# Optimization experiments

Hardware: AMD Instinct MI355X
Metric: run time of the kernel (lower is better)

## Reference

```python
import jax, jax.numpy as jnp
import numpy as np

DIM = 1024
HEADS = 16
DIM_HEAD = 64
INNER = HEADS * DIM_HEAD
SCALE = DIM_HEAD ** -0.5


def setup_inputs() -> dict:
    key = jax.random.key(0)
    k1, k2, k3 = jax.random.split(key, 3)
    b, n = 2, 2048
    x = jax.random.normal(k1, (b, n, DIM), dtype=jnp.float32)
    mask = jnp.ones((b, n), dtype=bool)
    # to_qkv: Linear(dim, 3*inner, bias=False) stored as [dim, 3*inner]
    w_qkv = jax.random.normal(k2, (DIM, 3 * INNER), dtype=jnp.float32) * (DIM ** -0.5)
    # to_out: Linear(inner, dim, bias=False) stored as [inner, dim]
    w_out = jax.random.normal(k3, (INNER, DIM), dtype=jnp.float32) * (INNER ** -0.5)
    g = jnp.ones((DIM,), dtype=jnp.float32)  # LayerNorm gain
    return {"x": x, "mask": mask, "w_qkv": w_qkv, "w_out": w_out, "g": g}


def _layernorm(x, g):
    eps = 1e-5 if x.dtype == jnp.float32 else 1e-3
    mean = jnp.mean(x, axis=-1, keepdims=True)
    var = jnp.var(x, axis=-1, keepdims=True)  # unbiased=False
    return (x - mean) * jax.lax.rsqrt(var + eps) * g


def reference(x, mask, w_qkv, w_out, g):
    b, n, _ = x.shape
    qkv = x @ w_qkv  # [b, n, 3*inner]
    q, k, v = jnp.split(qkv, 3, axis=-1)
    # b n (h d) -> b h n d
    split_heads = lambda t: t.reshape(b, n, HEADS, DIM_HEAD).transpose(0, 2, 1, 3)
    q, k, v = split_heads(q), split_heads(k), split_heads(v)
    q = q * SCALE
    sim = jnp.einsum('bhid,bhjd->bhij', q, k)  # [b, h, n, n]
    mask_value = -jnp.finfo(sim.dtype).max
    key_mask = mask[:, None, None, :]  # b 1 1 j
    sim = jnp.where(key_mask, sim, mask_value)
    causal_mask = jnp.triu(jnp.ones((n, n), dtype=bool), k=1)
    sim = jnp.where(causal_mask, mask_value, sim)
    attn = jax.nn.softmax(sim.astype(jnp.float32), axis=-1).astype(sim.dtype)
    out = jnp.einsum('bhij,bhjd->bhid', attn, v)
    out = out.transpose(0, 2, 1, 3).reshape(b, n, INNER)  # b h n d -> b n (h d)
    out = out @ w_out
    return _layernorm(out, g)
```

## Files before the change

### kernel.cpp

```cpp
#include <hip/hip_runtime.h>
#include <hip/hip_bf16.h>


typedef __bf16 bf16_t;
typedef __bf16 bf16x8 __attribute__((ext_vector_type(8)));
typedef __bf16 bf16x4 __attribute__((ext_vector_type(4)));
typedef float  f32x4  __attribute__((ext_vector_type(4)));

#define DIMX   1024
#define HEADS  16
#define DHEAD  64
#define INNER  1024
#define SEQ    2048
#define BATCH  2
#define NROWS  (BATCH * SEQ)
#define QKV_N  (3 * INNER)
#define NQT    (SEQ / 64)
#define QK2SCALE 0.18033688011f

__device__ __forceinline__ bf16_t f2b(float f) { return (bf16_t)f; }

__device__ __forceinline__ float fexp2(float x) {
#if __has_builtin(__builtin_amdgcn_exp2f)
  return __builtin_amdgcn_exp2f(x);
#else
  return exp2f(x);
#endif
}

__device__ __forceinline__ void gload16(const bf16_t* g, bf16_t* s) {
  __builtin_amdgcn_global_load_lds(
      (const __attribute__((address_space(1))) unsigned int*)g,
      (__attribute__((address_space(3))) unsigned int*)s, 16, 0, 0);
}

__device__ __forceinline__ f32x4 mfma16(bf16x8 a, bf16x8 b, f32x4 c) {
  return __builtin_amdgcn_mfma_f32_16x16x32_bf16(a, b, c, 0, 0, 0);
}

__global__ __launch_bounds__(256)
void prep_all(const float* __restrict__ x, const float* __restrict__ w_qkv,
              const float* __restrict__ w_out, bf16_t* __restrict__ xb,
              bf16_t* __restrict__ wqkvT, bf16_t* __restrict__ woutT) {
  __shared__ float tile[32][33];
  const int bid = blockIdx.x;
  if (bid < 4096) {
    const int i = bid * 256 + threadIdx.x;
    float4 v = *(const float4*)&x[(size_t)i * 4];
    bf16x4 o;
    o[0] = f2b(v.x); o[1] = f2b(v.y); o[2] = f2b(v.z); o[3] = f2b(v.w);
    *(bf16x4*)&xb[(size_t)i * 4] = o;
    return;
  }
  const float* in; bf16_t* out; int R, C, bx, by;
  if (bid < 4096 + 3072) {
    const int t1 = bid - 4096;
    in = w_qkv; out = wqkvT; R = DIMX; C = QKV_N; bx = t1 % 96; by = t1 / 96;
  } else {
    const int t2 = bid - 7168;
    in = w_out; out = woutT; R = DIMX; C = DIMX; bx = t2 & 31; by = t2 >> 5;
  }
  const int c0 = bx * 32, r0 = by * 32;
  const int tx = threadIdx.x & 31, ty = threadIdx.x >> 5;
  #pragma unroll
  for (int i = 0; i < 32; i += 8)
    tile[ty + i][tx] = in[(size_t)(r0 + ty + i) * C + c0 + tx];
  __syncthreads();
  #pragma unroll
  for (int i = 0; i < 32; i += 8)
    out[(size_t)(c0 + ty + i) * R + r0 + tx] = f2b(tile[tx][ty + i]);
}

__global__ __launch_bounds__(256)
void vtrans(const bf16_t* __restrict__ qkv, bf16_t* __restrict__ vt) {
  __shared__ bf16_t t[64][66];
  const int bh = blockIdx.y;
  const int b = bh >> 4, h = bh & 15;
  const int j0 = blockIdx.x * 64;
  const int tx = threadIdx.x & 63, ty = threadIdx.x >> 6;
  #pragma unroll
  for (int i = 0; i < 64; i += 4)
    t[ty + i][tx] = qkv[(size_t)(b * SEQ + j0 + ty + i) * QKV_N + 2 * INNER + h * 64 + tx];
  __syncthreads();
  #pragma unroll
  for (int i = 0; i < 64; i += 4)
    vt[((size_t)bh * 64 + ty + i) * SEQ + j0 + tx] = t[tx][ty + i];
}

template<int OUT_F32>
__global__ __launch_bounds__(256)
void gemm_bt(const bf16_t* __restrict__ A, const bf16_t* __restrict__ Bt,
             void* __restrict__ Cp, int M, int N, int K) {
  constexpr int BK = 64;
  __shared__ bf16_t As[128 * BK];
  __shared__ bf16_t Bs[128 * BK];
  const int t = threadIdx.x;
  const int w = t >> 6, l = t & 63, lo = l & 15, hi = l >> 4;
  const int nwg = gridDim.x * gridDim.y;
  int flat = blockIdx.y * gridDim.x + blockIdx.x;
  if ((nwg & 7) == 0) flat = (flat & 7) * (nwg >> 3) + (flat >> 3);
  const int m0 = (flat / gridDim.x) * 128, n0 = (flat % gridDim.x) * 128;
  const int wm = (w >> 1) * 64, wn = (w & 1) * 64;
  const int sl  = l >> 3;
  const int sgc = ((l & 7) ^ sl) * 8;
  const int r7  = lo & 7;
  f32x4 acc[4][4] = {};
  for (int k0 = 0; k0 < K; k0 += BK) {
    #pragma unroll
    for (int c = 0; c < 4; ++c) {
      const int rb = w * 32 + c * 8;
      gload16(&A [(size_t)(m0 + rb + sl) * K + k0 + sgc], &As[rb * BK + l * 8]);
      gload16(&Bt[(size_t)(n0 + rb + sl) * K + k0 + sgc], &Bs[rb * BK + l * 8]);
    }
    __syncthreads();
    #pragma unroll
    for (int kk = 0; kk < 2; ++kk) {
      bf16x8 af[4], bfr[4];
      #pragma unroll
      for (int mi = 0; mi < 4; ++mi)
        af[mi] = *(const bf16x8*)&As[(wm + mi * 16 + lo) * BK +
                                     (((kk * 4 + hi) ^ r7) << 3)];
      #pragma unroll
      for (int nj = 0; nj < 4; ++nj)
        bfr[nj] = *(const bf16x8*)&Bs[(wn + nj * 16 + lo) * BK +
                                      (((kk * 4 + hi) ^ r7) << 3)];
      __builtin_amdgcn_s_setprio(1);
      #pragma unroll
      for (int mi = 0; mi < 4; ++mi)
        #pragma unroll
        for (int nj = 0; nj < 4; ++nj)
          acc[mi][nj] = mfma16(af[mi], bfr[nj], acc[mi][nj]);
      __builtin_amdgcn_s_setprio(0);
    }
    __syncthreads();
  }
  #pragma unroll
  for (int mi = 0; mi < 4; ++mi)
    #pragma unroll
    for (int nj = 0; nj < 4; ++nj)
      #pragma unroll
      for (int r = 0; r < 4; ++r) {
        size_t row = m0 + wm + mi * 16 + hi * 4 + r;
        size_t col = n0 + wn + nj * 16 + lo;
        if (OUT_F32)
          ((float*)Cp)[row * N + col] = acc[mi][nj][r];
        else
          ((bf16_t*)Cp)[row * N + col] = f2b(acc[mi][nj][r]);
      }
}

__global__ __launch_bounds__(256, 4)
void attn_fa12(const bf16_t* __restrict__ qkv, const bf16_t* __restrict__ vt,
               bf16_t* __restrict__ attn_out, bf16_t* __restrict__ pacc,
               float* __restrict__ plsum) {
  const int bx  = blockIdx.x;
  const int xcd = bx & 7, idx = bx >> 3;
  const int bh  = xcd * 4 + (idx & 3);
  const int ta  = (idx >> 2) & 15;
  const int half = idx >> 6;
  const int tb  = NQT - 1 - ta;
  const int b = bh >> 4, h = bh & 15;
  const int t = threadIdx.x, w = t >> 6, l = t & 63, lo = l & 15, hi = l >> 4;

  __shared__ bf16_t Ks[2][64 * 64];
  __shared__ bf16_t Vs[2][64 * 64];

  const int srow = l >> 3;
  const int sgc  = ((l & 7) ^ srow) * 8;
  const size_t kgbase = (size_t)(b * SEQ) * QKV_N + INNER + h * 64;
  const size_t vgbase = (size_t)bh * 64 * SEQ;

  auto STAGE = [&](int ti, int buf) {
    const int j0 = ti * 64;
    #pragma unroll
    for (int c = 0; c < 2; ++c) {
      const int rb = w * 16 + c * 8;
      gload16(&qkv[kgbase + (size_t)(j0 + rb + srow) * QKV_N + sgc],
              &Ks[buf][rb * 64]);
      gload16(&vt[vgbase + (size_t)(rb + srow) * SEQ + j0 + sgc],
              &Vs[buf][rb * 64]);
    }
  };

  const int r7 = lo & 7;
  bf16x8 vone8;
  #pragma unroll
  for (int i = 0; i < 8; ++i) vone8[i] = f2b(1.0f);
  f32x4 acc[4];
  f32x4 acc_l;

  auto SEG = [&](const int qt, const int t0, const int t1, const bool dmask) {
    const size_t qb = (size_t)(b * SEQ + qt * 64 + w * 16 + lo) * QKV_N + h * 64;
    bf16x8 qf0 = *(const bf16x8*)&qkv[qb + hi * 8];
    bf16x8 qf1 = *(const bf16x8*)&qkv[qb + 32 + hi * 8];
    #pragma unroll
    for (int i = 0; i < 8; ++i) {
      qf0[i] = f2b((float)qf0[i] * QK2SCALE);
      qf1[i] = f2b((float)qf1[i] * QK2SCALE);
    }
    const f32x4 fz = {};
    acc[0] = fz; acc[1] = fz; acc[2] = fz; acc[3] = fz;
    acc_l = fz;
    const int qrow = qt * 64 + w * 16 + lo;

    STAGE(t0, 0);
    for (int ti = t0; ti <= t1; ++ti) {
      const int buf = (ti - t0) & 1;
      __syncthreads();
      if (ti + 1 <= t1) STAGE(ti + 1, buf ^ 1);
      const bool mB = dmask && (ti == t1);
      __builtin_amdgcn_s_setprio(1);
      #pragma unroll
      for (int pr = 0; pr < 2; ++pr) {
        const int jb0 = pr * 2;
        if (!(mB && jb0 > w)) {
          bf16x8 pa;
          #pragma unroll
          for (int q = 0; q < 2; ++q) {
            const int jb = jb0 + q;
            f32x4 z = fz;
            if (!(mB && jb > w)) {
              const bf16_t* kp = &Ks[buf][(jb * 16 + lo) * 64];
              bf16x8 kf0 = *(const bf16x8*)&kp[(hi ^ r7) << 3];
              bf16x8 kf1 = *(const bf16x8*)&kp[((hi + 4) ^ r7) << 3];
              z = mfma16(kf0, qf0, z);
              z = mfma16(kf1, qf1, z);
            }
            #pragma unroll
            for (int r = 0; r < 4; ++r) {
              float pe = fexp2(z[r]);
              if (mB) {
                const int jglob = ti * 64 + jb * 16 + hi * 4 + r;
                if (jglob > qrow) pe = 0.f;
              }
              pa[q * 4 + r] = f2b(pe);
            }
          }
          #pragma unroll
          for (int dj = 0; dj < 4; ++dj) {
            const bf16_t* vp = &Vs[buf][(dj * 16 + lo) * 64];
            bf16x4 va = *(const bf16x4*)&vp[
                (((2 * jb0 + (hi >> 1)) ^ r7) << 3) + ((hi & 1) << 2)];
            bf16x4 vb = *(const bf16x4*)&vp[
                (((2 * jb0 + 2 + (hi >> 1)) ^ r7) << 3) + ((hi & 1) << 2)];
            bf16x8 vf;
            #pragma unroll
            for (int i = 0; i < 4; ++i) { vf[i] = va[i]; vf[i + 4] = vb[i]; }
            acc[dj] = mfma16(pa, vf, acc[dj]);
          }
          acc_l = mfma16(pa, vone8, acc_l);
        }
      }
      __builtin_amdgcn_s_setprio(0);
    }
    __syncthreads();
  };

  if (half == 0) {
    SEG(ta, 0, ta, true);
    #pragma unroll
    for (int r = 0; r < 4; ++r) {
      const float lr = 1.f / acc_l[r];
      #pragma unroll
      for (int dj = 0; dj < 4; ++dj)
        attn_out[(size_t)(b * SEQ + ta * 64 + w * 16 + hi * 4 + r) * INNER +
                 h * 64 + dj * 16 + lo] = f2b(acc[dj][r] * lr);
    }
    SEG(tb, 0, 15 - ta, false);
    {
      const int prb = (bh * 16 + (tb - 16)) * 64;
      #pragma unroll
      for (int dj = 0; dj < 4; ++dj)
        #pragma unroll
        for (int r = 0; r < 4; ++r)
          pacc[(size_t)(prb + w * 16 + hi * 4 + r) * 64 + dj * 16 + lo] =
              f2b(acc[dj][r]);
      if (lo == 0) {
        #pragma unroll
        for (int r = 0; r < 4; ++r)
          plsum[prb + w * 16 + hi * 4 + r] = acc_l[r];
      }
    }
  } else {
    SEG(tb, 16 - ta, tb, true);
    {
      const int prb = (bh * 16 + (tb - 16)) * 64;
      #pragma unroll
      for (int dj = 0; dj < 4; ++dj)
        #pragma unroll
        for (int r = 0; r < 4; ++r)
          pacc[2097152 + (size_t)(prb + w * 16 + hi * 4 + r) * 64 + dj * 16 + lo] =
              f2b(acc[dj][r]);
      if (lo == 0) {
        #pragma unroll
        for (int r = 0; r < 4; ++r)
          plsum[32768 + prb + w * 16 + hi * 4 + r] = acc_l[r];
      }
    }
  }
}

__global__ __launch_bounds__(256)
void attn_combine(const bf16_t* __restrict__ pacc, const float* __restrict__ plsum,
                  bf16_t* __restrict__ attn_out) {
  const int g = blockIdx.x * 256 + threadIdx.x;
  const int d8 = g & 7;
  const int row = g >> 3;
  const int qr = row & 63, qt = 16 + ((row >> 6) & 15), bh = row >> 10;
  const int b = bh >> 4, h = bh & 15;
  bf16x8 xa = *(const bf16x8*)&pacc[(size_t)row * 64 + d8 * 8];
  bf16x8 ya = *(const bf16x8*)&pacc[2097152 + (size_t)row * 64 + d8 * 8];
  const float inv = 1.f / (plsum[row] + plsum[32768 + row]);
  bf16x8 o;
  #pragma unroll
  for (int i = 0; i < 8; ++i)
    o[i] = f2b(((float)xa[i] + (float)ya[i]) * inv);
  *(bf16x8*)&attn_out[(size_t)(b * SEQ + qt * 64 + qr) * INNER + h * 64 + d8 * 8] = o;
}

__global__ __launch_bounds__(256)
void layernorm_b(const bf16_t* __restrict__ in, const float* __restrict__ g,
                 float* __restrict__ out) {
  const int row = blockIdx.x;
  const bf16_t* xr = in + (size_t)row * DIMX;
  const int c = threadIdx.x * 4;
  bf16x4 v4 = *(const bf16x4*)&xr[c];
  const float vx = (float)v4[0], vy = (float)v4[1], vz = (float)v4[2], vw = (float)v4[3];
  float s = vx + vy + vz + vw;
  float q = vx * vx + vy * vy + vz * vz + vw * vw;
  #pragma unroll
  for (int o = 32; o > 0; o >>= 1) {
    s += __shfl_down(s, o);
    q += __shfl_down(q, o);
  }
  __shared__ float rs[4], rq[4];
  const int wid = threadIdx.x >> 6;
  if ((threadIdx.x & 63) == 0) { rs[wid] = s; rq[wid] = q; }
  __syncthreads();
  s = rs[0] + rs[1] + rs[2] + rs[3];
  q = rq[0] + rq[1] + rq[2] + rq[3];
  const float mean = s * (1.f / DIMX);
  const float var  = q * (1.f / DIMX) - mean * mean;
  const float inv  = rsqrtf(var + 1e-5f);
  float4 gv = *(const float4*)&g[c];
  float4 o4;
  o4.x = (vx - mean) * inv * gv.x;
  o4.y = (vy - mean) * inv * gv.y;
  o4.z = (vz - mean) * inv * gv.z;
  o4.w = (vw - mean) * inv * gv.w;
  *(float4*)&out[(size_t)row * DIMX + c] = o4;
}

extern "C" void kernel_launch(void* const* d_in, const int* in_sizes, int n_in,
                              void* d_out, int out_size, void* d_ws, size_t ws_size,
                              hipStream_t stream) {
  const float* x     = (const float*)d_in[0];
  const float* w_qkv = (const float*)d_in[2];
  const float* w_out = (const float*)d_in[3];
  const float* g     = (const float*)d_in[4];

  char* ws = (char*)d_ws;
  const size_t MB = 1024 * 1024;
  bf16_t* xb     = (bf16_t*)(ws);
  bf16_t* wqkvT  = (bf16_t*)(ws + 8 * MB);
  bf16_t* woutT  = (bf16_t*)(ws + 14 * MB);
  bf16_t* qkv    = (bf16_t*)(ws + 16 * MB);
  bf16_t* vt     = (bf16_t*)(ws + 40 * MB);
  bf16_t* attn_o = (bf16_t*)(ws + 48 * MB);
  bf16_t* pacc   = (bf16_t*)(ws);
  float*  plsum  = (float*) (ws + 8 * MB);
  bf16_t* outpre = (bf16_t*)(ws + 16 * MB);

  prep_all<<<8192, 256, 0, stream>>>(x, w_qkv, w_out, xb, wqkvT, woutT);

  gemm_bt<0><<<dim3(QKV_N / 128, NROWS / 128), 256, 0, stream>>>(
      xb, wqkvT, qkv, NROWS, QKV_N, DIMX);

  vtrans<<<dim3(SEQ / 64, BATCH * HEADS), 256, 0, stream>>>(qkv, vt);

  attn_fa12<<<dim3(1024), 256, 0, stream>>>(qkv, vt, attn_o, pacc, plsum);
  attn_combine<<<dim3(1024), 256, 0, stream>>>(pacc, plsum, attn_o);

  gemm_bt<0><<<dim3(DIMX / 128, NROWS / 128), 256, 0, stream>>>(
      attn_o, woutT, outpre, NROWS, DIMX, DIMX);

  layernorm_b<<<NROWS, 256, 0, stream>>>(outpre, g, (float*)d_out);
}
```

Before: 112.4 us.

## Fuse V transpose into QKV GEMM epilogue and split-K the output projection

The QKV GEMM now writes V tiles transposed through shared memory straight into the vt buffer, which removes the separate vtrans kernel and its extra pass over V. The output projection is split into two K halves (grid z=2) so 512 workgroups run instead of 256, writing fp32 partials. LayerNorm then sums the two partials before normalizing. This trades one fewer launch and better occupancy for the projection against extra fp32 partial-buffer traffic (2x16MB write and read).

```diff
diff --git a/kernel.cpp b/kernel.cpp
--- a/kernel.cpp
+++ b/kernel.cpp
@@ -72,33 +72,17 @@
 }
 
 __global__ __launch_bounds__(256)
-void vtrans(const bf16_t* __restrict__ qkv, bf16_t* __restrict__ vt) {
-  __shared__ bf16_t t[64][66];
-  const int bh = blockIdx.y;
-  const int b = bh >> 4, h = bh & 15;
-  const int j0 = blockIdx.x * 64;
-  const int tx = threadIdx.x & 63, ty = threadIdx.x >> 6;
-  #pragma unroll
-  for (int i = 0; i < 64; i += 4)
-    t[ty + i][tx] = qkv[(size_t)(b * SEQ + j0 + ty + i) * QKV_N + 2 * INNER + h * 64 + tx];
-  __syncthreads();
-  #pragma unroll
-  for (int i = 0; i < 64; i += 4)
-    vt[((size_t)bh * 64 + ty + i) * SEQ + j0 + tx] = t[tx][ty + i];
-}
-
-template<int OUT_F32>
-__global__ __launch_bounds__(256)
-void gemm_bt(const bf16_t* __restrict__ A, const bf16_t* __restrict__ Bt,
-             void* __restrict__ Cp, int M, int N, int K) {
-  constexpr int BK = 64;
-  __shared__ bf16_t As[128 * BK];
-  __shared__ bf16_t Bs[128 * BK];
+void gemm_qkv(const bf16_t* __restrict__ A, const bf16_t* __restrict__ Bt,
+              bf16_t* __restrict__ C, bf16_t* __restrict__ vt) {
+  constexpr int BK = 64, K = 1024, N = QKV_N;
+  __shared__ bf16_t smem[2 * 128 * BK];
+  bf16_t* As = smem;
+  bf16_t* Bs = smem + 128 * BK;
   const int t = threadIdx.x;
   const int w = t >> 6, l = t & 63, lo = l & 15, hi = l >> 4;
   const int nwg = gridDim.x * gridDim.y;
   int flat = blockIdx.y * gridDim.x + blockIdx.x;
-  if ((nwg & 7) == 0) flat = (flat & 7) * (nwg >> 3) + (flat >> 3);
+  flat = (flat & 7) * (nwg >> 3) + (flat >> 3);
   const int m0 = (flat / gridDim.x) * 128, n0 = (flat % gridDim.x) * 128;
   const int wm = (w >> 1) * 64, wn = (w & 1) * 64;
   const int sl  = l >> 3;
@@ -134,19 +118,106 @@
     }
     __syncthreads();
   }
+  if (n0 < 2 * INNER) {
+    #pragma unroll
+    for (int mi = 0; mi < 4; ++mi)
+      #pragma unroll
+      for (int nj = 0; nj < 4; ++nj)
+        #pragma unroll
+        for (int r = 0; r < 4; ++r)
+          C[(size_t)(m0 + wm + mi * 16 + hi * 4 + r) * N +
+            n0 + wn + nj * 16 + lo] = f2b(acc[mi][nj][r]);
+  } else {
+    #pragma unroll
+    for (int mi = 0; mi < 4; ++mi)
+      #pragma unroll
+      for (int nj = 0; nj < 4; ++nj) {
+        const int cloc = wn + nj * 16 + lo;
+        const int g    = ((wm + mi * 16) >> 2) + hi;
+        bf16x4 pk;
+        #pragma unroll
+        for (int r = 0; r < 4; ++r) pk[r] = f2b(acc[mi][nj][r]);
+        *(bf16x4*)((char*)smem + cloc * 256 + (((g ^ (cloc & 31))) << 3)) = pk;
+      }
+    __syncthreads();
+    const int b  = m0 >> 11;
+    const int j0 = m0 & (SEQ - 1);
+    const int vrb = b * 1024 + (n0 - 2 * INNER);
+    #pragma unroll
+    for (int p = 0; p < 8; ++p) {
+      const int c = p * 16 + w * 4 + hi;
+      const int c31 = c & 31;
+      bf16x4 a0 = *(const bf16x4*)((const char*)smem + c * 256 +
+                                   (((2 * lo) ^ c31) << 3));
+      bf16x4 a1 = *(const bf16x4*)((const char*)smem + c * 256 +
+                                   (((2 * lo + 1) ^ c31) << 3));
+      bf16x8 o;
+      #pragma unroll
+      for (int i = 0; i < 4; ++i) { o[i] = a0[i]; o[i + 4] = a1[i]; }
+      *(bf16x8*)&vt[(size_t)(vrb + c) * SEQ + j0 + lo * 8] = o;
+    }
+  }
+}
+
+__global__ __launch_bounds__(256)
+void gemm_osk(const bf16_t* __restrict__ A0, const bf16_t* __restrict__ Bt0,
+              float* __restrict__ P) {
+  constexpr int BK = 64, KH = 512, LDA = 1024, N = DIMX, M = NROWS;
+  __shared__ bf16_t smem[2 * 128 * BK];
+  bf16_t* As = smem;
+  bf16_t* Bs = smem + 128 * BK;
+  const int ks = blockIdx.z;
+  const bf16_t* A  = A0  + ks * KH;
+  const bf16_t* Bt = Bt0 + ks * KH;
+  float* Cp = P + (size_t)ks * M * N;
+  const int t = threadIdx.x;
+  const int w = t >> 6, l = t & 63, lo = l & 15, hi = l >> 4;
+  const int nwg = gridDim.x * gridDim.y;
+  int flat = blockIdx.y * gridDim.x + blockIdx.x;
+  flat = (flat & 7) * (nwg >> 3) + (flat >> 3);
+  const int m0 = (flat / gridDim.x) * 128, n0 = (flat % gridDim.x) * 128;
+  const int wm = (w >> 1) * 64, wn = (w & 1) * 64;
+  const int sl  = l >> 3;
+  const int sgc = ((l & 7) ^ sl) * 8;
+  const int r7  = lo & 7;
+  f32x4 acc[4][4] = {};
+  for (int k0 = 0; k0 < KH; k0 += BK) {
+    #pragma unroll
+    for (int c = 0; c < 4; ++c) {
+      const int rb = w * 32 + c * 8;
+      gload16(&A [(size_t)(m0 + rb + sl) * LDA + k0 + sgc], &As[rb * BK + l * 8]);
+      gload16(&Bt[(size_t)(n0 + rb + sl) * LDA + k0 + sgc], &Bs[rb * BK + l * 8]);
+    }
+    __syncthreads();
+    #pragma unroll
+    for (int kk = 0; kk < 2; ++kk) {
+      bf16x8 af[4], bfr[4];
+      #pragma unroll
+      for (int mi = 0; mi < 4; ++mi)
+        af[mi] = *(const bf16x8*)&As[(wm + mi * 16 + lo) * BK +
+                                     (((kk * 4 + hi) ^ r7) << 3)];
+      #pragma unroll
+      for (int nj = 0; nj < 4; ++nj)
+        bfr[nj] = *(const bf16x8*)&Bs[(wn + nj * 16 + lo) * BK +
+                                      (((kk * 4 + hi) ^ r7) << 3)];
+      __builtin_amdgcn_s_setprio(1);
+      #pragma unroll
+      for (int mi = 0; mi < 4; ++mi)
+        #pragma unroll
+        for (int nj = 0; nj < 4; ++nj)
+          acc[mi][nj] = mfma16(af[mi], bfr[nj], acc[mi][nj]);
+      __builtin_amdgcn_s_setprio(0);
+    }
+    __syncthreads();
+  }
   #pragma unroll
   for (int mi = 0; mi < 4; ++mi)
     #pragma unroll
     for (int nj = 0; nj < 4; ++nj)
       #pragma unroll
-      for (int r = 0; r < 4; ++r) {
-        size_t row = m0 + wm + mi * 16 + hi * 4 + r;
-        size_t col = n0 + wn + nj * 16 + lo;
-        if (OUT_F32)
-          ((float*)Cp)[row * N + col] = acc[mi][nj][r];
-        else
-          ((bf16_t*)Cp)[row * N + col] = f2b(acc[mi][nj][r]);
-      }
+      for (int r = 0; r < 4; ++r)
+        Cp[(size_t)(m0 + wm + mi * 16 + hi * 4 + r) * N +
+           n0 + wn + nj * 16 + lo] = acc[mi][nj][r];
 }
 
 __global__ __launch_bounds__(256, 4)
@@ -319,13 +390,13 @@
 }
 
 __global__ __launch_bounds__(256)
-void layernorm_b(const bf16_t* __restrict__ in, const float* __restrict__ g,
-                 float* __restrict__ out) {
+void layernorm_sk(const float* __restrict__ p0, const float* __restrict__ p1,
+                  const float* __restrict__ g, float* __restrict__ out) {
   const int row = blockIdx.x;
-  const bf16_t* xr = in + (size_t)row * DIMX;
   const int c = threadIdx.x * 4;
-  bf16x4 v4 = *(const bf16x4*)&xr[c];
-  const float vx = (float)v4[0], vy = (float)v4[1], vz = (float)v4[2], vw = (float)v4[3];
+  float4 a = *(const float4*)&p0[(size_t)row * DIMX + c];
+  float4 bq = *(const float4*)&p1[(size_t)row * DIMX + c];
+  const float vx = a.x + bq.x, vy = a.y + bq.y, vz = a.z + bq.z, vw = a.w + bq.w;
   float s = vx + vy + vz + vw;
   float q = vx * vx + vy * vy + vz * vz + vw * vw;
   #pragma unroll
@@ -369,20 +440,19 @@
   bf16_t* attn_o = (bf16_t*)(ws + 48 * MB);
   bf16_t* pacc   = (bf16_t*)(ws);
   float*  plsum  = (float*) (ws + 8 * MB);
-  bf16_t* outpre = (bf16_t*)(ws + 16 * MB);
+  float*  partP  = (float*) (ws + 16 * MB);
 
   prep_all<<<8192, 256, 0, stream>>>(x, w_qkv, w_out, xb, wqkvT, woutT);
 
-  gemm_bt<0><<<dim3(QKV_N / 128, NROWS / 128), 256, 0, stream>>>(
-      xb, wqkvT, qkv, NROWS, QKV_N, DIMX);
-
-  vtrans<<<dim3(SEQ / 64, BATCH * HEADS), 256, 0, stream>>>(qkv, vt);
+  gemm_qkv<<<dim3(QKV_N / 128, NROWS / 128), 256, 0, stream>>>(
+      xb, wqkvT, qkv, vt);
 
   attn_fa12<<<dim3(1024), 256, 0, stream>>>(qkv, vt, attn_o, pacc, plsum);
   attn_combine<<<dim3(1024), 256, 0, stream>>>(pacc, plsum, attn_o);
 
-  gemm_bt<0><<<dim3(DIMX / 128, NROWS / 128), 256, 0, stream>>>(
-      attn_o, woutT, outpre, NROWS, DIMX, DIMX);
-
-  layernorm_b<<<NROWS, 256, 0, stream>>>(outpre, g, (float*)d_out);
-}
+  gemm_osk<<<dim3(DIMX / 128, NROWS / 128, 2), 256, 0, stream>>>(
+      attn_o, woutT, partP);
+
+  layernorm_sk<<<NROWS, 256, 0, stream>>>(
+      partP, partP + (size_t)NROWS * DIMX, g, (float*)d_out);
+}
```

Result: faster. 107.1 us (-4.7%).
